# Kernel tuning notes

Hardware: AMD Instinct MI355X
Metric: run time of the kernel (lower is better)

Reference implementation:

```python
import jax, jax.numpy as jnp
import numpy as np

HIDDEN = 4096
N_HEADS = 32
N_KV_HEADS = 8
HEAD_DIM = 128
ROPE_BASE = 10000.0


def setup_inputs() -> dict:
    key = jax.random.key(0)
    k1, k2, k3, k4, k5 = jax.random.split(key, 5)
    s = 0.02  # init scale for weights
    return {
        "hidden_states": jax.random.normal(k1, (1, 2048, HIDDEN), dtype=jnp.float32),
        "Wq": jax.random.normal(k2, (N_HEADS * HEAD_DIM, HIDDEN), dtype=jnp.float32) * s,
        "Wk": jax.random.normal(k3, (N_KV_HEADS * HEAD_DIM, HIDDEN), dtype=jnp.float32) * s,
        "Wv": jax.random.normal(k4, (N_KV_HEADS * HEAD_DIM, HIDDEN), dtype=jnp.float32) * s,
        "Wo": jax.random.normal(k5, (HIDDEN, HIDDEN), dtype=jnp.float32) * s,
    }


def _rope(x, cos, sin):
    # x: [B, H, T, D]; cos/sin: [T, D/2] -> rotate split halves (Llama style)
    d2 = x.shape[-1] // 2
    x1, x2 = x[..., :d2], x[..., d2:]
    return jnp.concatenate([x1 * cos - x2 * sin, x1 * sin + x2 * cos], axis=-1)


def reference(hidden_states, Wq, Wk, Wv, Wo):
    B, T, _ = hidden_states.shape
    H, Hkv, D = N_HEADS, N_KV_HEADS, HEAD_DIM
    G = H // Hkv  # kv groups

    q = jnp.einsum("bth,qh->btq", hidden_states, Wq).reshape(B, T, H, D).transpose(0, 2, 1, 3)
    k = jnp.einsum("bth,kh->btk", hidden_states, Wk).reshape(B, T, Hkv, D).transpose(0, 2, 1, 3)
    v = jnp.einsum("bth,vh->btv", hidden_states, Wv).reshape(B, T, Hkv, D).transpose(0, 2, 1, 3)

    # RoPE (position_offset = 0)
    positions = jnp.arange(T, dtype=jnp.float32)
    inv_freq = ROPE_BASE ** (-jnp.arange(0, D, 2, dtype=jnp.float32) / D)  # [D/2]
    angles = positions[:, None] * inv_freq[None, :]                        # [T, D/2]
    cos, sin = jnp.cos(angles), jnp.sin(angles)
    q = _rope(q, cos, sin)
    k = _rope(k, cos, sin)

    # GQA attention without materializing expanded K/V: group query heads
    qg = q.reshape(B, Hkv, G, T, D)
    scale = 1.0 / jnp.sqrt(jnp.asarray(D, dtype=q.dtype))
    scores = jnp.einsum("bkgtd,bksd->bkgts", qg, k) * scale  # [B, Hkv, G, T, T]
    causal = jnp.tril(jnp.ones((T, T), dtype=bool))
    scores = jnp.where(causal, scores, jnp.finfo(scores.dtype).min)
    probs = jax.nn.softmax(scores, axis=-1)
    attn = jnp.einsum("bkgts,bksd->bkgtd", probs, v)          # [B, Hkv, G, T, D]
    attn = attn.reshape(B, H, T, D).transpose(0, 2, 1, 3).reshape(B, T, H * D)

    return jnp.einsum("btq,oq->bto", attn, Wo)
```

## Files before the change

### kernel.cpp

```cpp
#include <hip/hip_runtime.h>
#include <stdint.h>

#define T_SEQ   2048
#define HID     4096
#define NH      32
#define NKV     8
#define HD      128
#define QCOLS   6144
#define QK_SCALE 0.08838834764831845f

typedef _Float16 half_t;
typedef _Float16 half8 __attribute__((ext_vector_type(8)));
typedef _Float16 half4v __attribute__((ext_vector_type(4)));
typedef float    f32x4 __attribute__((ext_vector_type(4)));

typedef __attribute__((address_space(1))) const void cg_void;
typedef __attribute__((address_space(3))) void lds_void;

__global__ __launch_bounds__(256) void cast_all_k(const float* __restrict__ X,
                                                  const float* __restrict__ Wq,
                                                  const float* __restrict__ Wk,
                                                  const float* __restrict__ Wv,
                                                  const float* __restrict__ Wo,
                                                  half_t* __restrict__ Xh,
                                                  half_t* __restrict__ Wqkvh,
                                                  half_t* __restrict__ Woh) {
  int i = blockIdx.x * 256 + threadIdx.x;
  const float* src; half_t* dst; int off;
  if (i < 2097152)      { src = X;  dst = Xh;               off = i; }
  else if (i < 6291456) { src = Wq; dst = Wqkvh;            off = i - 2097152; }
  else if (i < 7340032) { src = Wk; dst = Wqkvh + 16777216; off = i - 6291456; }
  else if (i < 8388608) { src = Wv; dst = Wqkvh + 20971520; off = i - 7340032; }
  else                  { src = Wo; dst = Woh;              off = i - 8388608; }
  f32x4 v = *(const f32x4*)(src + (size_t)off * 4);
  half4v o;
  o[0] = (half_t)v[0]; o[1] = (half_t)v[1]; o[2] = (half_t)v[2]; o[3] = (half_t)v[3];
  *(half4v*)(dst + (size_t)off * 4) = o;
}

__global__ __launch_bounds__(256) void rope_tables_k(float* __restrict__ cs) {
  int idx = blockIdx.x * 256 + threadIdx.x;
  int t = idx >> 6, i = idx & 63;
  float inv = expf(-(float)i * 0.14391156831212787f);
  float a = (float)t * inv;
  cs[idx] = cosf(a);
  cs[131072 + idx] = sinf(a);
}

__global__ __launch_bounds__(256) void rope_apply_k(half_t* __restrict__ QKV,
                                                    const float* __restrict__ cs) {
  int idx = blockIdx.x * 256 + threadIdx.x;
  int i = idx & 63;
  int rem = idx >> 6;
  int head = rem % 40;
  int t = rem / 40;
  int colbase = (head < 32) ? head * HD : HID + (head - 32) * HD;
  size_t base = (size_t)t * QCOLS + colbase;
  float c = cs[t * 64 + i], s = cs[131072 + t * 64 + i];
  float x1 = (float)QKV[base + i];
  float x2 = (float)QKV[base + 64 + i];
  float o1 = x1 * c - x2 * s;
  float o2 = x1 * s + x2 * c;
  if (head < 32) { o1 *= QK_SCALE; o2 *= QK_SCALE; }
  QKV[base + i]      = (half_t)o1;
  QKV[base + 64 + i] = (half_t)o2;
}

__global__ __launch_bounds__(256) void transpose_v_k(const half_t* __restrict__ QKV,
                                                     half_t* __restrict__ Vt) {
  int idx = blockIdx.x * 256 + threadIdx.x;
  int d  = idx & 127;
  int ts = (idx >> 7) & 255;
  int kh = idx >> 15;
  half8 o;
#pragma unroll
  for (int i = 0; i < 8; ++i)
    o[i] = QKV[(size_t)(ts * 8 + i) * QCOLS + HID + NKV * HD + kh * HD + d];
  *(half8*)&Vt[(size_t)kh * (HD * T_SEQ) + (size_t)d * T_SEQ + ts * 8] = o;
}

template <int BM, int BN, int OUT_HALF>
__global__ __launch_bounds__(512, 2) void gemm8p_k(const half_t* __restrict__ A,
                                                   const half_t* __restrict__ Bm,
                                                   void* __restrict__ Cout,
                                                   int M, int N, int K) {
  constexpr int MF = BM / 32;
  constexpr int NF = BN / 64;
  constexpr int MH = MF / 2;
  constexpr int LA = BM / 64;
  constexpr int LB = BN / 64;
  __shared__ half_t Al[2][BM * 64];
  __shared__ half_t Bl[2][BN * 64];

  const int nbm = M / BM;
  const int nwg = nbm * (N / BN);
  const int bid = blockIdx.x;
  const int swz = (bid & 7) * (nwg >> 3) + (bid >> 3);
  const int brow = (swz % nbm) * BM;
  const int bcol = (swz / nbm) * BN;
  const int tid = threadIdx.x;
  const int lane = tid & 63, wid = tid >> 6;
  const int wr = wid >> 2, wc = wid & 3;
  const int lr = lane & 15, hi = lane >> 4;
  const int wrow = wr * (MF * 16), wcol = wc * (NF * 16);

  const half_t* Ab = A + (size_t)brow * K;
  const half_t* Bb = Bm + (size_t)bcol * K;

  f32x4 acc[MF][NF] = {};
  half8 afr[MH], bfr[NF];

#define STAGE_A(l, k0, buf) { \
    int c_ = (l) * 512 + tid; int r_ = c_ >> 3, s_ = c_ & 7; \
    __builtin_amdgcn_global_load_lds( \
      (cg_void*)(Ab + (size_t)r_ * K + (k0) + ((s_ ^ (r_ & 7)) * 8)), \
      (lds_void*)(&Al[buf][((l) * 512 + wid * 64) * 8]), 16, 0, 0); }
#define STAGE_B(l, k0, buf) { \
    int c_ = (l) * 512 + tid; int r_ = c_ >> 3, s_ = c_ & 7; \
    __builtin_amdgcn_global_load_lds( \
      (cg_void*)(Bb + (size_t)r_ * K + (k0) + ((s_ ^ (r_ & 7)) * 8)), \
      (lds_void*)(&Bl[buf][((l) * 512 + wid * 64) * 8]), 16, 0, 0); }
#define RD_A(i, mh, kk, buf) { \
    int row_ = wrow + ((mh) * MH + (i)) * 16 + lr; int ks_ = (kk) * 4 + hi; \
    afr[i] = *(const half8*)&Al[buf][row_ * 64 + ((ks_ ^ (row_ & 7)) * 8)]; }
#define RD_B(n, kk, buf) { \
    int row_ = wcol + (n) * 16 + lr; int ks_ = (kk) * 4 + hi; \
    bfr[n] = *(const half8*)&Bl[buf][row_ * 64 + ((ks_ ^ (row_ & 7)) * 8)]; }
#define MFMA_PH(mh) { \
    __builtin_amdgcn_s_setprio(1); \
    _Pragma("unroll") for (int i_ = 0; i_ < MH; ++i_) \
      _Pragma("unroll") for (int n_ = 0; n_ < NF; ++n_) \
        acc[(mh) * MH + i_][n_] = __builtin_amdgcn_mfma_f32_16x16x32_f16( \
            afr[i_], bfr[n_], acc[(mh) * MH + i_][n_], 0, 0, 0); \
    __builtin_amdgcn_s_setprio(0); }

#define DO_TILE(T, BUF) { \
    const int kn_ = ((T) + 1) * 64; const bool pf_ = ((T) + 1) < NT; \
     \
    if (pf_) { _Pragma("unroll") for (int l_ = 0; l_ < LA; ++l_) STAGE_A(l_, kn_, (BUF) ^ 1); } \
    _Pragma("unroll") for (int n_ = 0; n_ < NF; ++n_) RD_B(n_, 0, BUF); \
    _Pragma("unroll") for (int i_ = 0; i_ < MH; ++i_) RD_A(i_, 0, 0, BUF); \
    MFMA_PH(0); \
    __builtin_amdgcn_s_barrier(); __builtin_amdgcn_sched_barrier(0); \
     \
    if (pf_) { _Pragma("unroll") for (int l_ = 0; l_ < LB; ++l_) STAGE_B(l_, kn_, (BUF) ^ 1); } \
    _Pragma("unroll") for (int i_ = 0; i_ < MH; ++i_) RD_A(i_, 1, 0, BUF); \
    MFMA_PH(1); \
    __builtin_amdgcn_s_barrier(); __builtin_amdgcn_sched_barrier(0); \
     \
    _Pragma("unroll") for (int n_ = 0; n_ < NF; ++n_) RD_B(n_, 1, BUF); \
    _Pragma("unroll") for (int i_ = 0; i_ < MH; ++i_) RD_A(i_, 1, 1, BUF); \
    MFMA_PH(1); \
    __builtin_amdgcn_s_barrier(); __builtin_amdgcn_sched_barrier(0); \
     \
    _Pragma("unroll") for (int i_ = 0; i_ < MH; ++i_) RD_A(i_, 0, 1, BUF); \
    MFMA_PH(0); \
    asm volatile("s_waitcnt vmcnt(0)" ::: "memory"); \
    __syncthreads(); }

  const int NT = K / 64;
#pragma unroll
  for (int l_ = 0; l_ < LA; ++l_) STAGE_A(l_, 0, 0);
#pragma unroll
  for (int l_ = 0; l_ < LB; ++l_) STAGE_B(l_, 0, 0);
  asm volatile("s_waitcnt vmcnt(0)" ::: "memory");
  __syncthreads();

  for (int t = 0; t < NT; t += 2) {
    DO_TILE(t, 0);
    DO_TILE(t + 1, 1);
  }

#undef STAGE_A
#undef STAGE_B
#undef RD_A
#undef RD_B
#undef MFMA_PH
#undef DO_TILE

#pragma unroll
  for (int m = 0; m < MF; ++m)
#pragma unroll
    for (int n = 0; n < NF; ++n)
#pragma unroll
      for (int r = 0; r < 4; ++r) {
        int row = brow + wrow + m * 16 + hi * 4 + r;
        int col = bcol + wcol + n * 16 + lr;
        float v = acc[m][n][r];
        if (OUT_HALF) ((half_t*)Cout)[(size_t)row * N + col] = (half_t)v;
        else          ((float*)Cout)[(size_t)row * N + col] = v;
      }
}

__global__ __launch_bounds__(256, 2) void attn_k(const half_t* __restrict__ QKV,
                                                 const half_t* __restrict__ Vt,
                                                 half_t* __restrict__ Ob) {
  const int bid = blockIdx.x;
  const int qb = (bid < 256) ? (15 - (bid >> 5)) : ((bid - 256) >> 5);
  const int h  = bid & 31;
  const int kh = h >> 2;
  const int tid = threadIdx.x;
  const int lane = tid & 63;
  const int w = tid >> 6;
  const int lr = lane & 15, hi = lane >> 4;
  const int qbase = qb * 128;

  __shared__ half_t Klds[64 * 128];
  __shared__ half_t Vlds[128 * 64];
  __shared__ half_t Plds[4 * 32 * 72];

  const half_t* Qp  = QKV + h * HD;
  const half_t* Kp  = QKV + HID + kh * HD;
  const half_t* Vtp = Vt + (size_t)kh * (HD * T_SEQ);

  half8 qf[2][4];
#pragma unroll
  for (int s = 0; s < 2; ++s)
#pragma unroll
    for (int kk = 0; kk < 4; ++kk)
      qf[s][kk] = *(const half8*)&Qp[(size_t)(qbase + s * 64 + w * 16 + lr) * QCOLS + kk * 32 + hi * 8];

  f32x4 acc[2][8] = {};
  float mrow[2][4], lrow[2][4];
#pragma unroll
  for (int s = 0; s < 2; ++s)
#pragma unroll
    for (int r = 0; r < 4; ++r) { mrow[s][r] = -1e30f; lrow[s][r] = 0.0f; }

  half_t* Pw = &Plds[w * (32 * 72)];
  const int nt = 2 * qb + 2;
  for (int t = 0; t < nt; ++t) {
    const int kv0 = t * 64;
#pragma unroll
    for (int c = 0; c < 4; ++c) {
      int chunk = c * 256 + tid;
      int r = chunk >> 4, s = chunk & 15;
      int cc = (s & 8) | ((s ^ r) & 7);
      __builtin_amdgcn_global_load_lds(
          (cg_void*)(Kp + (size_t)(kv0 + r) * QCOLS + cc * 8),
          (lds_void*)(&Klds[(c * 256 + w * 64) * 8]), 16, 0, 0);
    }
#pragma unroll
    for (int c = 0; c < 4; ++c) {
      int chunk = c * 256 + tid;
      int r = chunk >> 3, s = chunk & 7;
      int cc = (s ^ r) & 7;
      __builtin_amdgcn_global_load_lds(
          (cg_void*)(Vtp + (size_t)r * T_SEQ + kv0 + cc * 8),
          (lds_void*)(&Vlds[(c * 256 + w * 64) * 8]), 16, 0, 0);
    }
    __syncthreads();

    f32x4 sc[2][4] = {};
#pragma unroll
    for (int jt = 0; jt < 4; ++jt)
#pragma unroll
      for (int kk = 0; kk < 4; ++kk) {
        int srow = jt * 16 + lr;
        int sl = kk * 4 + hi;
        int c = (sl & 8) | ((sl ^ srow) & 7);
        half8 kf = *(const half8*)&Klds[srow * 128 + c * 8];
        sc[0][jt] = __builtin_amdgcn_mfma_f32_16x16x32_f16(qf[0][kk], kf, sc[0][jt], 0, 0, 0);
        sc[1][jt] = __builtin_amdgcn_mfma_f32_16x16x32_f16(qf[1][kk], kf, sc[1][jt], 0, 0, 0);
      }

    if (t >= 2 * qb) {
#pragma unroll
      for (int s = 0; s < 2; ++s)
#pragma unroll
        for (int jt = 0; jt < 4; ++jt)
#pragma unroll
          for (int r = 0; r < 4; ++r) {
            int ig = qbase + s * 64 + w * 16 + hi * 4 + r;
            int jg = kv0 + jt * 16 + lr;
            if (jg > ig) sc[s][jt][r] = -1e30f;
          }
    }

#pragma unroll
    for (int s = 0; s < 2; ++s) {
      float mx[4], scl[4], ls[4];
#pragma unroll
      for (int r = 0; r < 4; ++r)
        mx[r] = fmaxf(fmaxf(sc[s][0][r], sc[s][1][r]), fmaxf(sc[s][2][r], sc[s][3][r]));
#pragma unroll
      for (int off = 1; off < 16; off <<= 1)
#pragma unroll
        for (int r = 0; r < 4; ++r)
          mx[r] = fmaxf(mx[r], __shfl_xor(mx[r], off, 64));
#pragma unroll
      for (int r = 0; r < 4; ++r) {
        float mn = fmaxf(mrow[s][r], mx[r]);
        scl[r] = __expf(mrow[s][r] - mn);
        mrow[s][r] = mn;
        ls[r] = 0.0f;
#pragma unroll
        for (int jt = 0; jt < 4; ++jt) {
          sc[s][jt][r] = __expf(sc[s][jt][r] - mn);
          ls[r] += sc[s][jt][r];
        }
      }
#pragma unroll
      for (int off = 1; off < 16; off <<= 1)
#pragma unroll
        for (int r = 0; r < 4; ++r)
          ls[r] += __shfl_xor(ls[r], off, 64);
#pragma unroll
      for (int r = 0; r < 4; ++r) lrow[s][r] = lrow[s][r] * scl[r] + ls[r];
#pragma unroll
      for (int g = 0; g < 8; ++g)
#pragma unroll
        for (int r = 0; r < 4; ++r) acc[s][g][r] *= scl[r];
    }

#pragma unroll
    for (int s = 0; s < 2; ++s)
#pragma unroll
      for (int jt = 0; jt < 4; ++jt)
#pragma unroll
        for (int r = 0; r < 4; ++r)
          Pw[(s * 16 + hi * 4 + r) * 72 + jt * 16 + lr] = (half_t)sc[s][jt][r];
    half8 pf[2][2];
#pragma unroll
    for (int s = 0; s < 2; ++s)
#pragma unroll
      for (int jt = 0; jt < 2; ++jt)
        pf[s][jt] = *(const half8*)&Pw[(s * 16 + lr) * 72 + jt * 32 + hi * 8];

#pragma unroll
    for (int g = 0; g < 8; ++g)
#pragma unroll
      for (int jt = 0; jt < 2; ++jt) {
        int vrow = g * 16 + lr;
        int sl = jt * 4 + hi;
        int c = (sl ^ vrow) & 7;
        half8 vf = *(const half8*)&Vlds[vrow * 64 + c * 8];
        acc[0][g] = __builtin_amdgcn_mfma_f32_16x16x32_f16(pf[0][jt], vf, acc[0][g], 0, 0, 0);
        acc[1][g] = __builtin_amdgcn_mfma_f32_16x16x32_f16(pf[1][jt], vf, acc[1][g], 0, 0, 0);
      }
    __syncthreads();
  }

#pragma unroll
  for (int s = 0; s < 2; ++s)
#pragma unroll
    for (int g = 0; g < 8; ++g)
#pragma unroll
      for (int r = 0; r < 4; ++r) {
        int row = qbase + s * 64 + w * 16 + hi * 4 + r;
        int col = h * HD + g * 16 + lr;
        Ob[(size_t)row * HID + col] = (half_t)(acc[s][g][r] / lrow[s][r]);
      }
}

extern "C" void kernel_launch(void* const* d_in, const int* in_sizes, int n_in,
                              void* d_out, int out_size, void* d_ws, size_t ws_size,
                              hipStream_t stream) {
  const float* hs = (const float*)d_in[0];
  const float* Wq = (const float*)d_in[1];
  const float* Wk = (const float*)d_in[2];
  const float* Wv = (const float*)d_in[3];
  const float* Wo = (const float*)d_in[4];
  float* out = (float*)d_out;

  char* ws = (char*)d_ws;
  half_t* Xh    = (half_t*)(ws + 0);
  half_t* Vt    = (half_t*)(ws + 0);
  half_t* Wqkvh = (half_t*)(ws + 16777216);
  half_t* Woh   = (half_t*)(ws + 67108864);
  half_t* QKV   = (half_t*)(ws + 100663296);
  half_t* attnh = (half_t*)(ws + 125829120);
  float*  cs    = (float*)(ws + 142606336);
  if (ws_size < 143654912ull) return;

  cast_all_k<<<49152, 256, 0, stream>>>(hs, Wq, Wk, Wv, Wo, Xh, Wqkvh, Woh);
  rope_tables_k<<<512, 256, 0, stream>>>(cs);

  gemm8p_k<256, 192, 1><<<256, 512, 0, stream>>>(Xh, Wqkvh, (void*)QKV, 2048, 6144, 4096);
  rope_apply_k<<<20480, 256, 0, stream>>>(QKV, cs);
  transpose_v_k<<<1024, 256, 0, stream>>>(QKV, Vt);
  attn_k<<<512, 256, 0, stream>>>(QKV, Vt, attnh);
  gemm8p_k<128, 256, 0><<<256, 512, 0, stream>>>(attnh, Woh, (void*)out, 2048, 4096, 4096);
}
```

Before: 336.2 us.

## Spread GEMM prefetch across phases with partial vmcnt waits instead of full drains

Reworks the double-buffered GEMM main loop so the next tile's global-to-LDS loads are split into chunks issued across the four MFMA phases. A-tile loads are reordered by half-tile so each phase only waits (via partial vmcnt counts) for the rows it is about to read. The old per-tile vmcnt(0) plus __syncthreads drain is removed and the last tile is peeled. The goal is to overlap memory loads with MFMA work and cut stalls, at the cost of fragile wait-count logic that assumes a specific load ordering and tile shape.

```diff
diff --git a/kernel.cpp b/kernel.cpp
--- a/kernel.cpp
+++ b/kernel.cpp
@@ -89,6 +89,11 @@
   constexpr int MH = MF / 2;
   constexpr int LA = BM / 64;
   constexpr int LB = BN / 64;
+  constexpr int LAH = LA / 2;
+  constexpr int L  = LA + LB;
+  constexpr int QBM4 = BM / 4;
+  constexpr int W1 = L - (LB + LAH);
+  constexpr int W2 = 2;
   __shared__ half_t Al[2][BM * 64];
   __shared__ half_t Bl[2][BN * 64];
 
@@ -110,16 +115,22 @@
   f32x4 acc[MF][NF] = {};
   half8 afr[MH], bfr[NF];
 
-#define STAGE_A(l, k0, buf) { \
-    int c_ = (l) * 512 + tid; int r_ = c_ >> 3, s_ = c_ & 7; \
+#define STAGE_B(l, k0, buf) { \
+    int c_ = (l) * 512 + tid; int r_ = c_ >> 3, sB_ = c_ & 7; \
     __builtin_amdgcn_global_load_lds( \
-      (cg_void*)(Ab + (size_t)r_ * K + (k0) + ((s_ ^ (r_ & 7)) * 8)), \
-      (lds_void*)(&Al[buf][((l) * 512 + wid * 64) * 8]), 16, 0, 0); }
-#define STAGE_B(l, k0, buf) { \
-    int c_ = (l) * 512 + tid; int r_ = c_ >> 3, s_ = c_ & 7; \
+      (cg_void*)(Bb + (size_t)r_ * K + (k0) + ((sB_ ^ (r_ & 7)) * 8)), \
+      (lds_void*)(&Bl[buf][((l) * 512 + wid * 64) * 8]), 16, 0, 0); }
+#define STAGE_AH(h, j, k0, buf) { \
+    int o0_ = (j) * 64 + wid * 8; \
+    int rb_ = (o0_ / QBM4) * (BM / 2) + (h) * QBM4 + (o0_ % QBM4); \
+    int rl_ = rb_ + (lane >> 3); int sA_ = lane & 7; \
     __builtin_amdgcn_global_load_lds( \
-      (cg_void*)(Bb + (size_t)r_ * K + (k0) + ((s_ ^ (r_ & 7)) * 8)), \
-      (lds_void*)(&Bl[buf][((l) * 512 + wid * 64) * 8]), 16, 0, 0); }
+      (cg_void*)(Ab + (size_t)rl_ * K + (k0) + ((sA_ ^ (rl_ & 7)) * 8)), \
+      (lds_void*)(&Al[buf][rb_ * 64]), 16, 0, 0); }
+#define STAGE_RANGE(Q0, Q1, kn, buf) { \
+    _Pragma("unroll") for (int q_ = (Q0); q_ < (Q1); ++q_) { \
+      if (q_ < LB) { STAGE_B(q_, (kn), (buf)); } \
+      else { int a_ = q_ - LB; STAGE_AH(a_ / LAH, a_ % LAH, (kn), (buf)); } } }
 #define RD_A(i, mh, kk, buf) { \
     int row_ = wrow + ((mh) * MH + (i)) * 16 + lr; int ks_ = (kk) * 4 + hi; \
     afr[i] = *(const half8*)&Al[buf][row_ * 64 + ((ks_ ^ (row_ & 7)) * 8)]; }
@@ -133,49 +144,52 @@
         acc[(mh) * MH + i_][n_] = __builtin_amdgcn_mfma_f32_16x16x32_f16( \
             afr[i_], bfr[n_], acc[(mh) * MH + i_][n_], 0, 0, 0); \
     __builtin_amdgcn_s_setprio(0); }
-
-#define DO_TILE(T, BUF) { \
-    const int kn_ = ((T) + 1) * 64; const bool pf_ = ((T) + 1) < NT; \
+#define PH_SYNC() { __builtin_amdgcn_s_barrier(); __builtin_amdgcn_sched_barrier(0); }
+
+#define DO_TILE(T, BUF, PF, W2X) { \
+    const int kn_ = ((T) + 1) * 64; \
      \
-    if (pf_) { _Pragma("unroll") for (int l_ = 0; l_ < LA; ++l_) STAGE_A(l_, kn_, (BUF) ^ 1); } \
+    asm volatile("s_waitcnt vmcnt(%0)" :: "n"(W1)); \
+    PH_SYNC(); \
+    if (PF) { STAGE_RANGE(0, 2, kn_, (BUF) ^ 1); } \
     _Pragma("unroll") for (int n_ = 0; n_ < NF; ++n_) RD_B(n_, 0, BUF); \
     _Pragma("unroll") for (int i_ = 0; i_ < MH; ++i_) RD_A(i_, 0, 0, BUF); \
     MFMA_PH(0); \
-    __builtin_amdgcn_s_barrier(); __builtin_amdgcn_sched_barrier(0); \
      \
-    if (pf_) { _Pragma("unroll") for (int l_ = 0; l_ < LB; ++l_) STAGE_B(l_, kn_, (BUF) ^ 1); } \
+    asm volatile("s_waitcnt vmcnt(%0)" :: "n"(W2X)); \
+    PH_SYNC(); \
+    if (PF) { STAGE_RANGE(2, 4, kn_, (BUF) ^ 1); } \
     _Pragma("unroll") for (int i_ = 0; i_ < MH; ++i_) RD_A(i_, 1, 0, BUF); \
     MFMA_PH(1); \
-    __builtin_amdgcn_s_barrier(); __builtin_amdgcn_sched_barrier(0); \
      \
+    PH_SYNC(); \
+    if (PF) { STAGE_RANGE(4, 6, kn_, (BUF) ^ 1); } \
     _Pragma("unroll") for (int n_ = 0; n_ < NF; ++n_) RD_B(n_, 1, BUF); \
     _Pragma("unroll") for (int i_ = 0; i_ < MH; ++i_) RD_A(i_, 1, 1, BUF); \
     MFMA_PH(1); \
-    __builtin_amdgcn_s_barrier(); __builtin_amdgcn_sched_barrier(0); \
      \
+    PH_SYNC(); \
+    if (PF) { STAGE_RANGE(6, L, kn_, (BUF) ^ 1); } \
     _Pragma("unroll") for (int i_ = 0; i_ < MH; ++i_) RD_A(i_, 0, 1, BUF); \
-    MFMA_PH(0); \
-    asm volatile("s_waitcnt vmcnt(0)" ::: "memory"); \
-    __syncthreads(); }
+    MFMA_PH(0); }
 
   const int NT = K / 64;
-#pragma unroll
-  for (int l_ = 0; l_ < LA; ++l_) STAGE_A(l_, 0, 0);
-#pragma unroll
-  for (int l_ = 0; l_ < LB; ++l_) STAGE_B(l_, 0, 0);
-  asm volatile("s_waitcnt vmcnt(0)" ::: "memory");
-  __syncthreads();
-
-  for (int t = 0; t < NT; t += 2) {
-    DO_TILE(t, 0);
-    DO_TILE(t + 1, 1);
+  STAGE_RANGE(0, L, 0, 0);
+
+  for (int t = 0; t < NT - 2; t += 2) {
+    DO_TILE(t, 0, 1, W2);
+    DO_TILE(t + 1, 1, 1, W2);
   }
-
-#undef STAGE_A
+  DO_TILE(NT - 2, 0, 1, W2);
+  DO_TILE(NT - 1, 1, 0, 0);
+
 #undef STAGE_B
+#undef STAGE_AH
+#undef STAGE_RANGE
 #undef RD_A
 #undef RD_B
 #undef MFMA_PH
+#undef PH_SYNC
 #undef DO_TILE
 
 #pragma unroll
```

After: 389.3 us. +15.8%, slower.

## Fuse RoPE and V-transpose launches; skip softmax rescale when max unchanged

Applied to the files above, without the earlier changes.

Merges the RoPE application and V transpose into one launch, with block ranges selecting the role, to save a launch. The two parts touch disjoint columns (Q/K versus V), so they can run concurrently. In the attention loop, the per-tile row-sum shuffle reduction moves to a single reduction after the loop, and the rescale of the accumulator and running sum is skipped when no lane's row max grew (wave-uniform via __any). The final division becomes a reciprocal multiply. This adds a divergent branch but removes redundant exps, shuffles and multiplies in the common case.

```diff
diff --git a/kernel.cpp b/kernel.cpp
--- a/kernel.cpp
+++ b/kernel.cpp
@@ -47,36 +47,36 @@
   cs[131072 + idx] = sinf(a);
 }
 
-__global__ __launch_bounds__(256) void rope_apply_k(half_t* __restrict__ QKV,
-                                                    const float* __restrict__ cs) {
-  int idx = blockIdx.x * 256 + threadIdx.x;
-  int i = idx & 63;
-  int rem = idx >> 6;
-  int head = rem % 40;
-  int t = rem / 40;
-  int colbase = (head < 32) ? head * HD : HID + (head - 32) * HD;
-  size_t base = (size_t)t * QCOLS + colbase;
-  float c = cs[t * 64 + i], s = cs[131072 + t * 64 + i];
-  float x1 = (float)QKV[base + i];
-  float x2 = (float)QKV[base + 64 + i];
-  float o1 = x1 * c - x2 * s;
-  float o2 = x1 * s + x2 * c;
-  if (head < 32) { o1 *= QK_SCALE; o2 *= QK_SCALE; }
-  QKV[base + i]      = (half_t)o1;
-  QKV[base + 64 + i] = (half_t)o2;
-}
-
-__global__ __launch_bounds__(256) void transpose_v_k(const half_t* __restrict__ QKV,
-                                                     half_t* __restrict__ Vt) {
-  int idx = blockIdx.x * 256 + threadIdx.x;
-  int d  = idx & 127;
-  int ts = (idx >> 7) & 255;
-  int kh = idx >> 15;
-  half8 o;
-#pragma unroll
-  for (int i = 0; i < 8; ++i)
-    o[i] = QKV[(size_t)(ts * 8 + i) * QCOLS + HID + NKV * HD + kh * HD + d];
-  *(half8*)&Vt[(size_t)kh * (HD * T_SEQ) + (size_t)d * T_SEQ + ts * 8] = o;
+__global__ __launch_bounds__(256) void rope_vt_k(half_t* __restrict__ QKV,
+                                                 const float* __restrict__ cs,
+                                                 half_t* __restrict__ Vt) {
+  if (blockIdx.x < 20480) {
+    int idx = blockIdx.x * 256 + threadIdx.x;
+    int i = idx & 63;
+    int rem = idx >> 6;
+    int head = rem % 40;
+    int t = rem / 40;
+    int colbase = (head < 32) ? head * HD : HID + (head - 32) * HD;
+    size_t base = (size_t)t * QCOLS + colbase;
+    float c = cs[t * 64 + i], s = cs[131072 + t * 64 + i];
+    float x1 = (float)QKV[base + i];
+    float x2 = (float)QKV[base + 64 + i];
+    float o1 = x1 * c - x2 * s;
+    float o2 = x1 * s + x2 * c;
+    if (head < 32) { o1 *= QK_SCALE; o2 *= QK_SCALE; }
+    QKV[base + i]      = (half_t)o1;
+    QKV[base + 64 + i] = (half_t)o2;
+  } else {
+    int idx = (blockIdx.x - 20480) * 256 + threadIdx.x;
+    int d  = idx & 127;
+    int ts = (idx >> 7) & 255;
+    int kh = idx >> 15;
+    half8 o;
+#pragma unroll
+    for (int i = 0; i < 8; ++i)
+      o[i] = QKV[(size_t)(ts * 8 + i) * QCOLS + HID + NKV * HD + kh * HD + d];
+    *(half8*)&Vt[(size_t)kh * (HD * T_SEQ) + (size_t)d * T_SEQ + ts * 8] = o;
+  }
 }
 
 template <int BM, int BN, int OUT_HALF>
@@ -136,23 +136,19 @@
 
 #define DO_TILE(T, BUF) { \
     const int kn_ = ((T) + 1) * 64; const bool pf_ = ((T) + 1) < NT; \
-     \
     if (pf_) { _Pragma("unroll") for (int l_ = 0; l_ < LA; ++l_) STAGE_A(l_, kn_, (BUF) ^ 1); } \
     _Pragma("unroll") for (int n_ = 0; n_ < NF; ++n_) RD_B(n_, 0, BUF); \
     _Pragma("unroll") for (int i_ = 0; i_ < MH; ++i_) RD_A(i_, 0, 0, BUF); \
     MFMA_PH(0); \
     __builtin_amdgcn_s_barrier(); __builtin_amdgcn_sched_barrier(0); \
-     \
     if (pf_) { _Pragma("unroll") for (int l_ = 0; l_ < LB; ++l_) STAGE_B(l_, kn_, (BUF) ^ 1); } \
     _Pragma("unroll") for (int i_ = 0; i_ < MH; ++i_) RD_A(i_, 1, 0, BUF); \
     MFMA_PH(1); \
     __builtin_amdgcn_s_barrier(); __builtin_amdgcn_sched_barrier(0); \
-     \
     _Pragma("unroll") for (int n_ = 0; n_ < NF; ++n_) RD_B(n_, 1, BUF); \
     _Pragma("unroll") for (int i_ = 0; i_ < MH; ++i_) RD_A(i_, 1, 1, BUF); \
     MFMA_PH(1); \
     __builtin_amdgcn_s_barrier(); __builtin_amdgcn_sched_barrier(0); \
-     \
     _Pragma("unroll") for (int i_ = 0; i_ < MH; ++i_) RD_A(i_, 0, 1, BUF); \
     MFMA_PH(0); \
     asm volatile("s_waitcnt vmcnt(0)" ::: "memory"); \
@@ -279,7 +275,7 @@
 
 #pragma unroll
     for (int s = 0; s < 2; ++s) {
-      float mx[4], scl[4], ls[4];
+      float mx[4];
 #pragma unroll
       for (int r = 0; r < 4; ++r)
         mx[r] = fmaxf(fmaxf(sc[s][0][r], sc[s][1][r]), fmaxf(sc[s][2][r], sc[s][3][r]));
@@ -288,29 +284,40 @@
 #pragma unroll
         for (int r = 0; r < 4; ++r)
           mx[r] = fmaxf(mx[r], __shfl_xor(mx[r], off, 64));
-#pragma unroll
-      for (int r = 0; r < 4; ++r) {
-        float mn = fmaxf(mrow[s][r], mx[r]);
-        scl[r] = __expf(mrow[s][r] - mn);
-        mrow[s][r] = mn;
-        ls[r] = 0.0f;
-#pragma unroll
-        for (int jt = 0; jt < 4; ++jt) {
-          sc[s][jt][r] = __expf(sc[s][jt][r] - mn);
-          ls[r] += sc[s][jt][r];
+      bool grow = false;
+#pragma unroll
+      for (int r = 0; r < 4; ++r) grow = grow || (mx[r] > mrow[s][r]);
+      if (__any(grow)) {
+        float scl[4];
+#pragma unroll
+        for (int r = 0; r < 4; ++r) {
+          float mn = fmaxf(mrow[s][r], mx[r]);
+          scl[r] = __expf(mrow[s][r] - mn);
+          mrow[s][r] = mn;
+          float ls = 0.0f;
+#pragma unroll
+          for (int jt = 0; jt < 4; ++jt) {
+            sc[s][jt][r] = __expf(sc[s][jt][r] - mn);
+            ls += sc[s][jt][r];
+          }
+          lrow[s][r] = lrow[s][r] * scl[r] + ls;
+        }
+#pragma unroll
+        for (int g = 0; g < 8; ++g)
+#pragma unroll
+          for (int r = 0; r < 4; ++r) acc[s][g][r] *= scl[r];
+      } else {
+#pragma unroll
+        for (int r = 0; r < 4; ++r) {
+          float ls = 0.0f;
+#pragma unroll
+          for (int jt = 0; jt < 4; ++jt) {
+            sc[s][jt][r] = __expf(sc[s][jt][r] - mrow[s][r]);
+            ls += sc[s][jt][r];
+          }
+          lrow[s][r] += ls;
         }
       }
-#pragma unroll
-      for (int off = 1; off < 16; off <<= 1)
-#pragma unroll
-        for (int r = 0; r < 4; ++r)
-          ls[r] += __shfl_xor(ls[r], off, 64);
-#pragma unroll
-      for (int r = 0; r < 4; ++r) lrow[s][r] = lrow[s][r] * scl[r] + ls[r];
-#pragma unroll
-      for (int g = 0; g < 8; ++g)
-#pragma unroll
-        for (int r = 0; r < 4; ++r) acc[s][g][r] *= scl[r];
     }
 
 #pragma unroll
@@ -341,6 +348,16 @@
     __syncthreads();
   }
 
+  float linv[2][4];
+#pragma unroll
+  for (int s = 0; s < 2; ++s)
+#pragma unroll
+    for (int r = 0; r < 4; ++r) {
+      float l = lrow[s][r];
+#pragma unroll
+      for (int off = 1; off < 16; off <<= 1) l += __shfl_xor(l, off, 64);
+      linv[s][r] = 1.0f / l;
+    }
 #pragma unroll
   for (int s = 0; s < 2; ++s)
 #pragma unroll
@@ -349,7 +366,7 @@
       for (int r = 0; r < 4; ++r) {
         int row = qbase + s * 64 + w * 16 + hi * 4 + r;
         int col = h * HD + g * 16 + lr;
-        Ob[(size_t)row * HID + col] = (half_t)(acc[s][g][r] / lrow[s][r]);
+        Ob[(size_t)row * HID + col] = (half_t)(acc[s][g][r] * linv[s][r]);
       }
 }
 
@@ -377,8 +394,7 @@
   rope_tables_k<<<512, 256, 0, stream>>>(cs);
 
   gemm8p_k<256, 192, 1><<<256, 512, 0, stream>>>(Xh, Wqkvh, (void*)QKV, 2048, 6144, 4096);
-  rope_apply_k<<<20480, 256, 0, stream>>>(QKV, cs);
-  transpose_v_k<<<1024, 256, 0, stream>>>(QKV, Vt);
+  rope_vt_k<<<21504, 256, 0, stream>>>(QKV, cs, Vt);
   attn_k<<<512, 256, 0, stream>>>(QKV, Vt, attnh);
   gemm8p_k<128, 256, 0><<<256, 512, 0, stream>>>(attnh, Woh, (void*)out, 2048, 4096, 4096);
 }
```

Result: slower. 343.3 us (+2.1%).
